# Kernel optimization log

Hardware: AMD Instinct MI355X
Metric: run time of the kernel (lower is better)

## Reference

```python
import jax, jax.numpy as jnp
import numpy as np

# Model hyperparameters (match init_kwargs)
NUM_HEADS = 12
KEY_SIZE = 64
VALUE_SIZE = 64
D_MODEL = 768
NUM_LAYERS = 4
FFW = 3072
B, T, L = 2, 32, 256
LN_EPS = 1e-5


def _layer_norm(x, scale, offset):
    m = jnp.mean(x, axis=-1, keepdims=True)
    v = jnp.mean(jnp.square(x - m), axis=-1, keepdims=True)
    return (x - m) * jax.lax.rsqrt(v + LN_EPS) * scale + offset


def _axial_attn(x, Wq, Wk, Wv, Wo, bo, mode):
    # x: [B, T, L, D]
    b, t, l, d = x.shape
    q = (x @ Wq).reshape(b, t, l, NUM_HEADS, KEY_SIZE)
    k = (x @ Wk).reshape(b, t, l, NUM_HEADS, KEY_SIZE)
    v = (x @ Wv).reshape(b, t, l, NUM_HEADS, VALUE_SIZE)
    inv_sqrt_d = KEY_SIZE ** (-0.5)
    if mode == 'time':
        logits = jnp.einsum('btlhd,bTlhd->blhtT', q, k) * inv_sqrt_d
        w = jax.nn.softmax(logits, axis=-1)
        a = jnp.einsum('blhtT,bTlhd->btlhd', w, v)
    else:  # space
        logits = jnp.einsum('btlhd,btLhd->bthlL', q, k) * inv_sqrt_d
        w = jax.nn.softmax(logits, axis=-1)
        a = jnp.einsum('bthlL,btLhd->btlhd', w, v)
    a = a.reshape(b, t, l, NUM_HEADS * VALUE_SIZE)
    return a @ Wo + bo


def _forward(input_embeddings, Wq_t, Wk_t, Wv_t, Wo_t, bo_t,
             Wq_s, Wk_s, Wv_s, Wo_s, bo_s,
             ln_t_scale, ln_t_bias, ln_s_scale, ln_s_bias,
             ln2_scale, ln2_bias, W1, b1, W2, b2):
    def block(h, p):
        (wq_t, wk_t, wv_t, wo_t, bot, wq_s, wk_s, wv_s, wo_s, bos,
         lts, ltb, lss, lsb, l2s, l2b, w1, bb1, w2, bb2) = p
        # time attention + residual
        x = _layer_norm(h, lts, ltb)
        h = h + _axial_attn(x, wq_t, wk_t, wv_t, wo_t, bot, 'time')
        # space attention + residual
        x = _layer_norm(h, lss, lsb)
        h = h + _axial_attn(x, wq_s, wk_s, wv_s, wo_s, bos, 'space')
        # FFN + residual
        x = _layer_norm(h, l2s, l2b)
        ff = jax.nn.gelu(x @ w1 + bb1) @ w2 + bb2
        return h + ff, None

    params = (Wq_t, Wk_t, Wv_t, Wo_t, bo_t, Wq_s, Wk_s, Wv_s, Wo_s, bo_s,
              ln_t_scale, ln_t_bias, ln_s_scale, ln_s_bias,
              ln2_scale, ln2_bias, W1, b1, W2, b2)
    h, _ = jax.lax.scan(block, input_embeddings, params)
    return h


def setup_inputs() -> dict:
    key = jax.random.key(0)
    ks = jax.random.split(key, 32)
    D, H, KD, VD, F, NL = D_MODEL, NUM_HEADS, KEY_SIZE, VALUE_SIZE, FFW, NUM_LAYERS
    init_scale = 2.0 / np.sqrt(NL)  # VarianceScaling scale used by the module
    s_in = np.sqrt(init_scale / D).astype(np.float32)   # fan_in = D
    s_out = np.sqrt(init_scale / (H * VD)).astype(np.float32)
    s_ffw2 = np.sqrt(init_scale / F).astype(np.float32)
    x = jax.random.normal(ks[0], (B, T, L, D), dtype=jnp.float32)
    def nrm(k, shape, s):
        return jax.random.normal(k, shape, dtype=jnp.float32) * s
    inp = {
        'input_embeddings': x,
        'Wq_t': nrm(ks[1], (NL, D, H * KD), s_in),
        'Wk_t': nrm(ks[2], (NL, D, H * KD), s_in),
        'Wv_t': nrm(ks[3], (NL, D, H * VD), s_in),
        'Wo_t': nrm(ks[4], (NL, H * VD, D), s_out),
        'bo_t': jnp.zeros((NL, D), jnp.float32),
        'Wq_s': nrm(ks[5], (NL, D, H * KD), s_in),
        'Wk_s': nrm(ks[6], (NL, D, H * KD), s_in),
        'Wv_s': nrm(ks[7], (NL, D, H * VD), s_in),
        'Wo_s': nrm(ks[8], (NL, H * VD, D), s_out),
        'bo_s': jnp.zeros((NL, D), jnp.float32),
        'ln_t_scale': jnp.ones((NL, D), jnp.float32),
        'ln_t_bias': jnp.zeros((NL, D), jnp.float32),
        'ln_s_scale': jnp.ones((NL, D), jnp.float32),
        'ln_s_bias': jnp.zeros((NL, D), jnp.float32),
        'ln2_scale': jnp.ones((NL, D), jnp.float32),
        'ln2_bias': jnp.zeros((NL, D), jnp.float32),
        'W1': nrm(ks[9], (NL, D, F), s_in),
        'b1': jnp.zeros((NL, F), jnp.float32),
        'W2': nrm(ks[10], (NL, F, D), s_ffw2),
        'b2': jnp.zeros((NL, D), jnp.float32),
    }
    return inp


def reference(input_embeddings, Wq_t, Wk_t, Wv_t, Wo_t, bo_t,
              Wq_s, Wk_s, Wv_s, Wo_s, bo_s,
              ln_t_scale, ln_t_bias, ln_s_scale, ln_s_bias,
              ln2_scale, ln2_bias, W1, b1, W2, b2):
    return _forward(input_embeddings, Wq_t, Wk_t, Wv_t, Wo_t, bo_t,
                    Wq_s, Wk_s, Wv_s, Wo_s, bo_s,
                    ln_t_scale, ln_t_bias, ln_s_scale, ln_s_bias,
                    ln2_scale, ln2_bias, W1, b1, W2, b2)
```

## Files before the change

### kernel.cpp

```cpp
#include <hip/hip_runtime.h>


using bf16x8 = __attribute__((ext_vector_type(8))) short;
using f32x4  = __attribute__((ext_vector_type(4))) float;

__device__ __forceinline__ f32x4 mfma_bf16(bf16x8 a, bf16x8 b, f32x4 c) {
  return __builtin_amdgcn_mfma_f32_16x16x32_bf16(a, b, c, 0, 0, 0);
}

__device__ __forceinline__ short f2bs(float f) {
  union { float f; unsigned u; } x; x.f = f;
  unsigned r = x.u + 0x7fffu + ((x.u >> 16) & 1u);
  return (short)(r >> 16);
}

__device__ __forceinline__ f32x4 fzero() {
  f32x4 v; v[0] = 0.f; v[1] = 0.f; v[2] = 0.f; v[3] = 0.f; return v;
}

__device__ __forceinline__ float quad16_max(float v) {
  v = fmaxf(v, __shfl_xor(v, 1));
  v = fmaxf(v, __shfl_xor(v, 2));
  v = fmaxf(v, __shfl_xor(v, 4));
  v = fmaxf(v, __shfl_xor(v, 8));
  return v;
}
__device__ __forceinline__ float quad16_sum(float v) {
  v += __shfl_xor(v, 1); v += __shfl_xor(v, 2);
  v += __shfl_xor(v, 4); v += __shfl_xor(v, 8);
  return v;
}

#define LSTR 40
template<int MODE>
__global__ __launch_bounds__(256) void gemm_bt(
    const short* __restrict__ A, const short* __restrict__ BT,
    const float* __restrict__ bias, const float* __restrict__ resid,
    float* __restrict__ outF, short* __restrict__ outB,
    int M, int N, int K, int nx)
{
  __shared__ __align__(16) short lA[2][128 * LSTR];
  __shared__ __align__(16) short lB[2][128 * LSTR];
  const int tid  = threadIdx.x;
  const int wave = tid >> 6, lane = tid & 63;
  const int quad = lane >> 4, l16 = lane & 15;
  const int wm = wave >> 1, wn = wave & 1;

  const unsigned flat = blockIdx.x;
  const unsigned su = flat >> 3;
  const unsigned nxu = (unsigned)nx;
  const unsigned xt = su % nxu;
  const unsigned yt = (flat & 7u) + 8u * (su / nxu);
  const long bm0 = (long)yt * 128;
  const long bn0 = (long)xt * 128;

  const int c0 = wave * 2;
  const int srow = lane >> 2;
  const int sg   = lane & 3;
  const long arow0 = bm0 + c0 * 16 + srow;
  const long brow0 = bn0 + c0 * 16 + srow;
  const int  skk   = sg * 8;
  const int wofs0 = (c0 * 16 + srow) * LSTR + sg * 8;
  const int wofs1 = wofs0 + 16 * LSTR;

  f32x4 acc[4][4];
#pragma unroll
  for (int i = 0; i < 4; ++i)
#pragma unroll
    for (int j = 0; j < 4; ++j) acc[i][j] = fzero();

  const int niter = K >> 5;

  bf16x8 sa0 = *(const bf16x8*)(A  + arow0 * K + skk);
  bf16x8 sa1 = *(const bf16x8*)(A  + (arow0 + 16) * K + skk);
  bf16x8 sb0 = *(const bf16x8*)(BT + brow0 * K + skk);
  bf16x8 sb1 = *(const bf16x8*)(BT + (brow0 + 16) * K + skk);
  *(bf16x8*)&lA[0][wofs0] = sa0;
  *(bf16x8*)&lA[0][wofs1] = sa1;
  *(bf16x8*)&lB[0][wofs0] = sb0;
  *(bf16x8*)&lB[0][wofs1] = sb1;
  __syncthreads();

  for (int k = 0; k < niter; ++k) {
    const int cur = k & 1, nxt = cur ^ 1;
    const bool more = (k + 1) < niter;
    if (more) {
      const long ko = (long)(k + 1) * 32 + skk;
      sa0 = *(const bf16x8*)(A  + arow0 * K + ko);
      sa1 = *(const bf16x8*)(A  + (arow0 + 16) * K + ko);
      sb0 = *(const bf16x8*)(BT + brow0 * K + ko);
      sb1 = *(const bf16x8*)(BT + (brow0 + 16) * K + ko);
    }
    bf16x8 a[4], b[4];
#pragma unroll
    for (int i = 0; i < 4; ++i)
      a[i] = *(const bf16x8*)&lA[cur][(wm * 64 + i * 16 + l16) * LSTR + quad * 8];
#pragma unroll
    for (int j = 0; j < 4; ++j)
      b[j] = *(const bf16x8*)&lB[cur][(wn * 64 + j * 16 + l16) * LSTR + quad * 8];
#pragma unroll
    for (int i = 0; i < 4; ++i)
#pragma unroll
      for (int j = 0; j < 4; ++j)
        acc[i][j] = mfma_bf16(a[i], b[j], acc[i][j]);
    if (more) {
      *(bf16x8*)&lA[nxt][wofs0] = sa0;
      *(bf16x8*)&lA[nxt][wofs1] = sa1;
      *(bf16x8*)&lB[nxt][wofs0] = sb0;
      *(bf16x8*)&lB[nxt][wofs1] = sb1;
      __syncthreads();
    }
  }

#pragma unroll
  for (int i = 0; i < 4; ++i)
#pragma unroll
    for (int j = 0; j < 4; ++j)
#pragma unroll
      for (int r = 0; r < 4; ++r) {
        long gr = bm0 + wm * 64 + i * 16 + quad * 4 + r;
        long gc = bn0 + wn * 64 + j * 16 + l16;
        size_t idx = (size_t)gr * N + gc;
        float v = acc[i][j][r];
        if (MODE == 0) {
          outB[idx] = f2bs(v);
        } else if (MODE == 1) {
          outF[idx] = v + bias[gc] + resid[idx];
        } else {
          float t = v + bias[gc];
          float g = 0.5f * t * (1.f + tanhf(0.7978845608f * (t + 0.044715f * t * t * t)));
          outB[idx] = f2bs(g);
        }
      }
}

__global__ __launch_bounds__(256) void ln_kernel(
    const float* __restrict__ h, const float* __restrict__ sc,
    const float* __restrict__ bi, short* __restrict__ out)
{
  const int row = blockIdx.x, tid = threadIdx.x;
  const float* hr = h + (long)row * 768;
  float x0 = hr[tid], x1 = hr[tid + 256], x2 = hr[tid + 512];
  __shared__ float red[4];
  float s = x0 + x1 + x2;
#pragma unroll
  for (int m = 32; m >= 1; m >>= 1) s += __shfl_xor(s, m);
  if ((tid & 63) == 0) red[tid >> 6] = s;
  __syncthreads();
  float mean = (red[0] + red[1] + red[2] + red[3]) * (1.f / 768.f);
  float d0 = x0 - mean, d1 = x1 - mean, d2 = x2 - mean;
  float q = d0 * d0 + d1 * d1 + d2 * d2;
#pragma unroll
  for (int m = 32; m >= 1; m >>= 1) q += __shfl_xor(q, m);
  __syncthreads();
  if ((tid & 63) == 0) red[tid >> 6] = q;
  __syncthreads();
  float var = (red[0] + red[1] + red[2] + red[3]) * (1.f / 768.f);
  float inv = rsqrtf(var + 1e-5f);
  long o = (long)row * 768;
  out[o + tid]       = f2bs(d0 * inv * sc[tid]       + bi[tid]);
  out[o + tid + 256] = f2bs(d1 * inv * sc[tid + 256] + bi[tid + 256]);
  out[o + tid + 512] = f2bs(d2 * inv * sc[tid + 512] + bi[tid + 512]);
}

struct TP8 { const float* src[8]; short* dst[8]; long sstride, dstride; };

__global__ __launch_bounds__(256) void transpose768_all(TP8 p)
{
  __shared__ float t[32][33];
  const int g = blockIdx.z >> 2, l = blockIdx.z & 3;
  const float* in = p.src[g] + (long)l * 768 * 768;
  short* out = p.dst[g] + (long)l * p.dstride;
  const int n0 = blockIdx.x * 32, k0 = blockIdx.y * 32;
  const int r = threadIdx.x >> 5, c = threadIdx.x & 31;
#pragma unroll
  for (int rr = 0; rr < 4; ++rr)
    t[r + rr * 8][c] = in[(long)(k0 + r + rr * 8) * 768 + n0 + c];
  __syncthreads();
#pragma unroll
  for (int rr = 0; rr < 4; ++rr)
    out[(long)(n0 + r + rr * 8) * 768 + k0 + c] = f2bs(t[c][r + rr * 8]);
}

__global__ __launch_bounds__(256) void transpose_w(
    const float* __restrict__ in0, short* __restrict__ out0, int Kd, int Nd)
{
  __shared__ float t[32][33];
  const float* in = in0 + (long)blockIdx.z * Kd * Nd;
  short* out = out0 + (long)blockIdx.z * Kd * Nd;
  const int n0 = blockIdx.x * 32, k0 = blockIdx.y * 32;
  const int r = threadIdx.x >> 5, c = threadIdx.x & 31;
#pragma unroll
  for (int rr = 0; rr < 4; ++rr)
    t[r + rr * 8][c] = in[(long)(k0 + r + rr * 8) * Nd + n0 + c];
  __syncthreads();
#pragma unroll
  for (int rr = 0; rr < 4; ++rr)
    out[(long)(n0 + r + rr * 8) * Kd + k0 + c] = f2bs(t[c][r + rr * 8]);
}

__global__ __launch_bounds__(256) void attn_space(
    const short* __restrict__ qkv, short* __restrict__ ao)
{
  __shared__ __align__(16) short VT[64 * 256];
  __shared__ __align__(16) short P[4][16 * 256];
  const int qt = blockIdx.x, hh = blockIdx.y, bt = blockIdx.z;
  const long tok0 = (long)bt * 256;
  const int tid = threadIdx.x, wave = tid >> 6, lane = tid & 63;
  const int quad = lane >> 4, l16 = lane & 15;

#pragma unroll
  for (int it = 0; it < 8; ++it) {
    int chunk = it * 256 + tid;
    int vl = chunk >> 3, d8 = (chunk & 7) * 8;
    bf16x8 v = *(const bf16x8*)(qkv + (tok0 + vl) * 2304 + 1536 + hh * 64 + d8);
#pragma unroll
    for (int e = 0; e < 8; ++e) VT[(d8 + e) * 256 + vl] = v[e];
  }

  const int qr = qt * 64 + wave * 16;
  bf16x8 qf[2];
#pragma unroll
  for (int kk = 0; kk < 2; ++kk)
    qf[kk] = *(const bf16x8*)(qkv + (tok0 + qr + l16) * 2304 + hh * 64 + kk * 32 + quad * 8);

  f32x4 S[16];
#pragma unroll
  for (int j = 0; j < 16; ++j) S[j] = fzero();
#pragma unroll
  for (int j = 0; j < 16; ++j)
#pragma unroll
    for (int kk = 0; kk < 2; ++kk) {
      bf16x8 kf = *(const bf16x8*)(qkv + (tok0 + j * 16 + l16) * 2304 + 768 + hh * 64 + kk * 32 + quad * 8);
      S[j] = mfma_bf16(qf[kk], kf, S[j]);
    }

#pragma unroll
  for (int r = 0; r < 4; ++r) {
    float m = -1e30f;
#pragma unroll
    for (int j = 0; j < 16; ++j) m = fmaxf(m, S[j][r]);
    m = quad16_max(m);
    float sum = 0.f;
#pragma unroll
    for (int j = 0; j < 16; ++j) {
      float e = __expf((S[j][r] - m) * 0.125f);
      S[j][r] = e; sum += e;
    }
    sum = quad16_sum(sum);
    float inv = 1.f / sum;
#pragma unroll
    for (int j = 0; j < 16; ++j)
      P[wave][(quad * 4 + r) * 256 + j * 16 + l16] = f2bs(S[j][r] * inv);
  }
  __syncthreads();

  f32x4 O[4];
#pragma unroll
  for (int jn = 0; jn < 4; ++jn) O[jn] = fzero();
  for (int kk = 0; kk < 8; ++kk) {
    bf16x8 pf = *(const bf16x8*)&P[wave][l16 * 256 + kk * 32 + quad * 8];
#pragma unroll
    for (int jn = 0; jn < 4; ++jn) {
      bf16x8 vf = *(const bf16x8*)&VT[(jn * 16 + l16) * 256 + kk * 32 + quad * 8];
      O[jn] = mfma_bf16(pf, vf, O[jn]);
    }
  }
#pragma unroll
  for (int jn = 0; jn < 4; ++jn)
#pragma unroll
    for (int r = 0; r < 4; ++r) {
      int row = qr + quad * 4 + r;
      ao[(tok0 + row) * 768 + hh * 64 + jn * 16 + l16] = f2bs(O[jn][r]);
    }
}

__global__ __launch_bounds__(64) void attn_time(
    const short* __restrict__ qkv, short* __restrict__ ao)
{
  __shared__ __align__(16) short VT[64 * 32];
  __shared__ __align__(16) short P[32 * 32];
  const int ll = blockIdx.x, hh = blockIdx.y, b = blockIdx.z;
  const int lane = threadIdx.x;
  const int quad = lane >> 4, l16 = lane & 15;
#define TOK(t) (((long)(b * 32 + (t))) * 256 + ll)

#pragma unroll
  for (int it = 0; it < 4; ++it) {
    int chunk = it * 64 + lane;
    int t = chunk >> 3, d8 = (chunk & 7) * 8;
    bf16x8 v = *(const bf16x8*)(qkv + TOK(t) * 2304 + 1536 + hh * 64 + d8);
#pragma unroll
    for (int e = 0; e < 8; ++e) VT[(d8 + e) * 32 + t] = v[e];
  }

  bf16x8 qf[2][2];
#pragma unroll
  for (int mi = 0; mi < 2; ++mi)
#pragma unroll
    for (int kk = 0; kk < 2; ++kk)
      qf[mi][kk] = *(const bf16x8*)(qkv + TOK(mi * 16 + l16) * 2304 + hh * 64 + kk * 32 + quad * 8);

  f32x4 S[2][2];
#pragma unroll
  for (int mi = 0; mi < 2; ++mi) { S[mi][0] = fzero(); S[mi][1] = fzero(); }
#pragma unroll
  for (int nj = 0; nj < 2; ++nj)
#pragma unroll
    for (int kk = 0; kk < 2; ++kk) {
      bf16x8 kf = *(const bf16x8*)(qkv + TOK(nj * 16 + l16) * 2304 + 768 + hh * 64 + kk * 32 + quad * 8);
#pragma unroll
      for (int mi = 0; mi < 2; ++mi)
        S[mi][nj] = mfma_bf16(qf[mi][kk], kf, S[mi][nj]);
    }

#pragma unroll
  for (int mi = 0; mi < 2; ++mi)
#pragma unroll
    for (int r = 0; r < 4; ++r) {
      float m = fmaxf(S[mi][0][r], S[mi][1][r]);
      m = quad16_max(m);
      float e0 = __expf((S[mi][0][r] - m) * 0.125f);
      float e1 = __expf((S[mi][1][r] - m) * 0.125f);
      float sum = quad16_sum(e0 + e1);
      float inv = 1.f / sum;
      P[(mi * 16 + quad * 4 + r) * 32 + l16]      = f2bs(e0 * inv);
      P[(mi * 16 + quad * 4 + r) * 32 + 16 + l16] = f2bs(e1 * inv);
    }
  __syncthreads();

  f32x4 O[2][4];
#pragma unroll
  for (int mi = 0; mi < 2; ++mi)
#pragma unroll
    for (int jn = 0; jn < 4; ++jn) O[mi][jn] = fzero();
#pragma unroll
  for (int mi = 0; mi < 2; ++mi) {
    bf16x8 pf = *(const bf16x8*)&P[(mi * 16 + l16) * 32 + quad * 8];
#pragma unroll
    for (int jn = 0; jn < 4; ++jn) {
      bf16x8 vf = *(const bf16x8*)&VT[(jn * 16 + l16) * 32 + quad * 8];
      O[mi][jn] = mfma_bf16(pf, vf, O[mi][jn]);
    }
  }
#pragma unroll
  for (int mi = 0; mi < 2; ++mi)
#pragma unroll
    for (int jn = 0; jn < 4; ++jn)
#pragma unroll
      for (int r = 0; r < 4; ++r) {
        int t = mi * 16 + quad * 4 + r;
        ao[TOK(t) * 768 + hh * 64 + jn * 16 + l16] = f2bs(O[mi][jn][r]);
      }
#undef TOK
}

extern "C" void kernel_launch(void* const* d_in, const int* in_sizes, int n_in,
                              void* d_out, int out_size, void* d_ws, size_t ws_size,
                              hipStream_t stream)
{
  const float* emb     = (const float*)d_in[0];
  const float* Wq_t    = (const float*)d_in[1];
  const float* Wk_t    = (const float*)d_in[2];
  const float* Wv_t    = (const float*)d_in[3];
  const float* Wo_t    = (const float*)d_in[4];
  const float* bo_t    = (const float*)d_in[5];
  const float* Wq_s    = (const float*)d_in[6];
  const float* Wk_s    = (const float*)d_in[7];
  const float* Wv_s    = (const float*)d_in[8];
  const float* Wo_s    = (const float*)d_in[9];
  const float* bo_s    = (const float*)d_in[10];
  const float* ln_t_sc = (const float*)d_in[11];
  const float* ln_t_bi = (const float*)d_in[12];
  const float* ln_s_sc = (const float*)d_in[13];
  const float* ln_s_bi = (const float*)d_in[14];
  const float* ln2_sc  = (const float*)d_in[15];
  const float* ln2_bi  = (const float*)d_in[16];
  const float* W1      = (const float*)d_in[17];
  const float* b1      = (const float*)d_in[18];
  const float* W2      = (const float*)d_in[19];
  const float* b2      = (const float*)d_in[20];

  const long M = 16384, D = 768, QN = 2304, F = 3072;
  char* ws = (char*)d_ws;
  size_t off = 0;
  auto alloc = [&](size_t b) { char* p = ws + off; off += (b + 255) & ~(size_t)255; return p; };
  short* qkvT_t = (short*)alloc((size_t)4 * QN * D * 2);
  short* qkvT_s = (short*)alloc((size_t)4 * QN * D * 2);
  short* woT_t  = (short*)alloc((size_t)4 * D * D * 2);
  short* woT_s  = (short*)alloc((size_t)4 * D * D * 2);
  short* w1T    = (short*)alloc((size_t)4 * F * D * 2);
  short* w2T    = (short*)alloc((size_t)4 * D * F * 2);
  short* xb     = (short*)alloc((size_t)M * D * 2);
  short* aob    = (short*)alloc((size_t)M * D * 2);
  short* big    = (short*)alloc((size_t)M * F * 2);
  float* h = (float*)d_out;

  hipMemcpyAsync(h, emb, (size_t)M * D * 4, hipMemcpyDeviceToDevice, stream);

  TP8 tp;
  tp.src[0] = Wq_t; tp.dst[0] = qkvT_t;
  tp.src[1] = Wk_t; tp.dst[1] = qkvT_t + D * D;
  tp.src[2] = Wv_t; tp.dst[2] = qkvT_t + 2 * D * D;
  tp.src[3] = Wq_s; tp.dst[3] = qkvT_s;
  tp.src[4] = Wk_s; tp.dst[4] = qkvT_s + D * D;
  tp.src[5] = Wv_s; tp.dst[5] = qkvT_s + 2 * D * D;
  tp.src[6] = Wo_t; tp.dst[6] = woT_t;
  tp.src[7] = Wo_s; tp.dst[7] = woT_s;
  tp.sstride = D * D;
  tp.dstride = 0;
  TP8 tp_a = tp; tp_a.dstride = QN * D;
  TP8 tp_b = tp; tp_b.dstride = D * D;
  {
    transpose768_all<<<dim3(24, 24, 24), 256, 0, stream>>>(tp_a);
    TP8 tp_c;
    tp_c.src[0] = Wo_t; tp_c.dst[0] = woT_t;
    tp_c.src[1] = Wo_s; tp_c.dst[1] = woT_s;
    for (int g = 2; g < 8; ++g) { tp_c.src[g] = Wo_t; tp_c.dst[g] = woT_t; }
    tp_c.sstride = D * D; tp_c.dstride = D * D;
    transpose768_all<<<dim3(24, 24, 8), 256, 0, stream>>>(tp_c);
  }
  transpose_w<<<dim3(96, 24, 4), 256, 0, stream>>>(W1, w1T, 768, 3072);
  transpose_w<<<dim3(24, 96, 4), 256, 0, stream>>>(W2, w2T, 3072, 768);

  for (int l = 0; l < 4; ++l) {
    ln_kernel<<<16384, 256, 0, stream>>>(h, ln_t_sc + l * 768, ln_t_bi + l * 768, xb);
    gemm_bt<0><<<18 * 128, 256, 0, stream>>>(xb, qkvT_t + (long)l * QN * D,
        nullptr, nullptr, nullptr, big, 16384, 2304, 768, 18);
    attn_time<<<dim3(256, 12, 2), 64, 0, stream>>>(big, aob);
    gemm_bt<1><<<6 * 128, 256, 0, stream>>>(aob, woT_t + (long)l * D * D,
        bo_t + l * 768, h, h, nullptr, 16384, 768, 768, 6);
    ln_kernel<<<16384, 256, 0, stream>>>(h, ln_s_sc + l * 768, ln_s_bi + l * 768, xb);
    gemm_bt<0><<<18 * 128, 256, 0, stream>>>(xb, qkvT_s + (long)l * QN * D,
        nullptr, nullptr, nullptr, big, 16384, 2304, 768, 18);
    attn_space<<<dim3(4, 12, 64), 256, 0, stream>>>(big, aob);
    gemm_bt<1><<<6 * 128, 256, 0, stream>>>(aob, woT_s + (long)l * D * D,
        bo_s + l * 768, h, h, nullptr, 16384, 768, 768, 6);
    ln_kernel<<<16384, 256, 0, stream>>>(h, ln2_sc + l * 768, ln2_bi + l * 768, xb);
    gemm_bt<2><<<24 * 128, 256, 0, stream>>>(xb, w1T + (long)l * F * D,
        b1 + l * 3072, nullptr, nullptr, big, 16384, 3072, 768, 24);
    gemm_bt<1><<<6 * 128, 256, 0, stream>>>(big, w2T + (long)l * D * F,
        b2 + l * 768, h, h, nullptr, 16384, 768, 3072, 6);
  }
}
```

Before: 2.878 ms.

## Load GEMM B operand directly from global into registers, stage only A in LDS

```diff
diff --git a/kernel.cpp b/kernel.cpp
--- a/kernel.cpp
+++ b/kernel.cpp
@@ -31,7 +31,10 @@
   return v;
 }
 
-#define LSTR 40
+#define LSTR 72
+#define ABUF (128 * LSTR)
+#define ABUFB (ABUF * 2)
+
 template<int MODE>
 __global__ __launch_bounds__(256) void gemm_bt(
     const short* __restrict__ A, const short* __restrict__ BT,
@@ -39,8 +42,7 @@
     float* __restrict__ outF, short* __restrict__ outB,
     int M, int N, int K, int nx)
 {
-  __shared__ __align__(16) short lA[2][128 * LSTR];
-  __shared__ __align__(16) short lB[2][128 * LSTR];
+  __shared__ __align__(16) short lA[2 * ABUF];
   const int tid  = threadIdx.x;
   const int wave = tid >> 6, lane = tid & 63;
   const int quad = lane >> 4, l16 = lane & 15;
@@ -54,14 +56,20 @@
   const long bm0 = (long)yt * 128;
   const long bn0 = (long)xt * 128;
 
-  const int c0 = wave * 2;
-  const int srow = lane >> 2;
-  const int sg   = lane & 3;
-  const long arow0 = bm0 + c0 * 16 + srow;
-  const long brow0 = bn0 + c0 * 16 + srow;
-  const int  skk   = sg * 8;
-  const int wofs0 = (c0 * 16 + srow) * LSTR + sg * 8;
-  const int wofs1 = wofs0 + 16 * LSTR;
+  int voffA[4];
+#pragma unroll
+  for (int t = 0; t < 4; ++t)
+    voffA[t] = (int)(((bm0 + wave * 32 + t * 8 + (lane >> 3)) * (long)K
+                      + (lane & 7) * 8) * 2);
+  int voffB[4];
+#pragma unroll
+  for (int j = 0; j < 4; ++j)
+    voffB[j] = (int)(((bn0 + wn * 64 + j * 16 + l16) * (long)K + quad * 8) * 2);
+  const int ldsWr = ((wave * 32 + (lane >> 3)) * LSTR + (lane & 7) * 8) * 2;
+  const int ldsRd = ((wm * 64 + l16) * LSTR + quad * 8) * 2;
+
+  const char* aP = (const char*)A;
+  const char* bP = (const char*)BT;
 
   f32x4 acc[4][4];
 #pragma unroll
@@ -69,48 +77,72 @@
 #pragma unroll
     for (int j = 0; j < 4; ++j) acc[i][j] = fzero();
 
-  const int niter = K >> 5;
-
-  bf16x8 sa0 = *(const bf16x8*)(A  + arow0 * K + skk);
-  bf16x8 sa1 = *(const bf16x8*)(A  + (arow0 + 16) * K + skk);
-  bf16x8 sb0 = *(const bf16x8*)(BT + brow0 * K + skk);
-  bf16x8 sb1 = *(const bf16x8*)(BT + (brow0 + 16) * K + skk);
-  *(bf16x8*)&lA[0][wofs0] = sa0;
-  *(bf16x8*)&lA[0][wofs1] = sa1;
-  *(bf16x8*)&lB[0][wofs0] = sb0;
-  *(bf16x8*)&lB[0][wofs1] = sb1;
-  __syncthreads();
-
-  for (int k = 0; k < niter; ++k) {
-    const int cur = k & 1, nxt = cur ^ 1;
-    const bool more = (k + 1) < niter;
-    if (more) {
-      const long ko = (long)(k + 1) * 32 + skk;
-      sa0 = *(const bf16x8*)(A  + arow0 * K + ko);
-      sa1 = *(const bf16x8*)(A  + (arow0 + 16) * K + ko);
-      sb0 = *(const bf16x8*)(BT + brow0 * K + ko);
-      sb1 = *(const bf16x8*)(BT + (brow0 + 16) * K + ko);
-    }
-    bf16x8 a[4], b[4];
-#pragma unroll
-    for (int i = 0; i < 4; ++i)
-      a[i] = *(const bf16x8*)&lA[cur][(wm * 64 + i * 16 + l16) * LSTR + quad * 8];
-#pragma unroll
-    for (int j = 0; j < 4; ++j)
-      b[j] = *(const bf16x8*)&lB[cur][(wn * 64 + j * 16 + l16) * LSTR + quad * 8];
-#pragma unroll
-    for (int i = 0; i < 4; ++i)
-#pragma unroll
-      for (int j = 0; j < 4; ++j)
-        acc[i][j] = mfma_bf16(a[i], b[j], acc[i][j]);
-    if (more) {
-      *(bf16x8*)&lA[nxt][wofs0] = sa0;
-      *(bf16x8*)&lA[nxt][wofs1] = sa1;
-      *(bf16x8*)&lB[nxt][wofs0] = sb0;
-      *(bf16x8*)&lB[nxt][wofs1] = sb1;
-      __syncthreads();
-    }
-  }
+  const int niter = K >> 6;
+  bf16x8 astg[4], bc0[4], bc1[4];
+
+#pragma unroll
+  for (int t = 0; t < 4; ++t)
+    astg[t] = *(const bf16x8*)(aP + voffA[t]);
+#pragma unroll
+  for (int t = 0; t < 4; ++t)
+    *(bf16x8*)((char*)lA + ldsWr + t * 1152) = astg[t];
+#pragma unroll
+  for (int t = 0; t < 4; ++t)
+    astg[t] = *(const bf16x8*)(aP + 128 + voffA[t]);
+#pragma unroll
+  for (int j = 0; j < 4; ++j)
+    bc0[j] = *(const bf16x8*)(bP + voffB[j]);
+  __syncthreads();
+
+#define GEMM_ITER(BUF)                                                       \
+  {                                                                          \
+    const bool more1 = (k + 1) < niter;                                      \
+    const bool more2 = (k + 2) < niter;                                      \
+                          \
+    _Pragma("unroll")                                                        \
+    for (int j = 0; j < 4; ++j)                                              \
+      bc1[j] = *(const bf16x8*)(bP + voffB[j] + 64);                         \
+    bf16x8 a[4];                                                             \
+    _Pragma("unroll")                                                        \
+    for (int i = 0; i < 4; ++i)                                              \
+      a[i] = *(const bf16x8*)((char*)lA + (BUF)*ABUFB + ldsRd + i * 2304);   \
+    _Pragma("unroll")                                                        \
+    for (int i = 0; i < 4; ++i)                                              \
+      _Pragma("unroll")                                                      \
+      for (int j = 0; j < 4; ++j)                                            \
+        acc[i][j] = mfma_bf16(a[i], bc0[j], acc[i][j]);                      \
+    if (more1) {                                                             \
+      _Pragma("unroll")                                                      \
+      for (int t = 0; t < 4; ++t)                                            \
+        *(bf16x8*)((char*)lA + (1 - (BUF)) * ABUFB + ldsWr + t * 1152) =     \
+            astg[t];                                                         \
+      if (more2) {                                                           \
+        _Pragma("unroll")                                                    \
+        for (int t = 0; t < 4; ++t)                                          \
+          astg[t] = *(const bf16x8*)(aP + 256 + voffA[t]);                   \
+      }                                                                      \
+      _Pragma("unroll")                                                      \
+      for (int j = 0; j < 4; ++j)                                            \
+        bc0[j] = *(const bf16x8*)(bP + 128 + voffB[j]);                      \
+    }                                                                        \
+    _Pragma("unroll")                                                        \
+    for (int i = 0; i < 4; ++i)                                              \
+      a[i] = *(const bf16x8*)((char*)lA + (BUF)*ABUFB + ldsRd + i * 2304 + 64);\
+    _Pragma("unroll")                                                        \
+    for (int i = 0; i < 4; ++i)                                              \
+      _Pragma("unroll")                                                      \
+      for (int j = 0; j < 4; ++j)                                            \
+        acc[i][j] = mfma_bf16(a[i], bc1[j], acc[i][j]);                      \
+    if (more1) __syncthreads();                                              \
+    aP += 128; bP += 128; ++k;                                               \
+  }
+
+  int k = 0;
+  while (k < niter) {
+    GEMM_ITER(0)
+    GEMM_ITER(1)
+  }
+#undef GEMM_ITER
 
 #pragma unroll
   for (int i = 0; i < 4; ++i)
@@ -398,28 +430,24 @@
 
   hipMemcpyAsync(h, emb, (size_t)M * D * 4, hipMemcpyDeviceToDevice, stream);
 
-  TP8 tp;
-  tp.src[0] = Wq_t; tp.dst[0] = qkvT_t;
-  tp.src[1] = Wk_t; tp.dst[1] = qkvT_t + D * D;
-  tp.src[2] = Wv_t; tp.dst[2] = qkvT_t + 2 * D * D;
-  tp.src[3] = Wq_s; tp.dst[3] = qkvT_s;
-  tp.src[4] = Wk_s; tp.dst[4] = qkvT_s + D * D;
-  tp.src[5] = Wv_s; tp.dst[5] = qkvT_s + 2 * D * D;
-  tp.src[6] = Wo_t; tp.dst[6] = woT_t;
-  tp.src[7] = Wo_s; tp.dst[7] = woT_s;
-  tp.sstride = D * D;
-  tp.dstride = 0;
-  TP8 tp_a = tp; tp_a.dstride = QN * D;
-  TP8 tp_b = tp; tp_b.dstride = D * D;
-  {
-    transpose768_all<<<dim3(24, 24, 24), 256, 0, stream>>>(tp_a);
-    TP8 tp_c;
-    tp_c.src[0] = Wo_t; tp_c.dst[0] = woT_t;
-    tp_c.src[1] = Wo_s; tp_c.dst[1] = woT_s;
-    for (int g = 2; g < 8; ++g) { tp_c.src[g] = Wo_t; tp_c.dst[g] = woT_t; }
-    tp_c.sstride = D * D; tp_c.dstride = D * D;
-    transpose768_all<<<dim3(24, 24, 8), 256, 0, stream>>>(tp_c);
-  }
+  TP8 tp_a;
+  tp_a.src[0] = Wq_t; tp_a.dst[0] = qkvT_t;
+  tp_a.src[1] = Wk_t; tp_a.dst[1] = qkvT_t + D * D;
+  tp_a.src[2] = Wv_t; tp_a.dst[2] = qkvT_t + 2 * D * D;
+  tp_a.src[3] = Wq_s; tp_a.dst[3] = qkvT_s;
+  tp_a.src[4] = Wk_s; tp_a.dst[4] = qkvT_s + D * D;
+  tp_a.src[5] = Wv_s; tp_a.dst[5] = qkvT_s + 2 * D * D;
+  tp_a.src[6] = Wo_t; tp_a.dst[6] = woT_t;
+  tp_a.src[7] = Wo_s; tp_a.dst[7] = woT_s;
+  tp_a.sstride = D * D;
+  tp_a.dstride = QN * D;
+  transpose768_all<<<dim3(24, 24, 24), 256, 0, stream>>>(tp_a);
+  TP8 tp_c;
+  tp_c.src[0] = Wo_t; tp_c.dst[0] = woT_t;
+  tp_c.src[1] = Wo_s; tp_c.dst[1] = woT_s;
+  for (int g = 2; g < 8; ++g) { tp_c.src[g] = Wo_t; tp_c.dst[g] = woT_t; }
+  tp_c.sstride = D * D; tp_c.dstride = D * D;
+  transpose768_all<<<dim3(24, 24, 8), 256, 0, stream>>>(tp_c);
   transpose_w<<<dim3(96, 24, 4), 256, 0, stream>>>(W1, w1T, 768, 3072);
   transpose_w<<<dim3(24, 96, 4), 256, 0, stream>>>(W2, w2T, 3072, 768);
 
```

After: 3.715 ms. 29.0% more time.
